# Performance work log

Hardware: AMD Instinct MI355X
Metric: run time of the kernel (lower is better)

The kernel has to match this reference:

```python
import jax, jax.numpy as jnp
import numpy as np

TOP_K = 8


def setup_inputs() -> dict:
    key = jax.random.key(0)
    k1, k2 = jax.random.split(key)
    N, D, E = 16384, 4096, 64
    x = jax.random.normal(k1, (N, D), dtype=jnp.float32)
    W = jax.random.normal(k2, (E, D), dtype=jnp.float32) * (1.0 / np.sqrt(D))
    b = jnp.zeros((E,), dtype=jnp.float32)
    return {"x": x, "W": W, "b": b}


def reference(x, W, b):
    # gate: [N, E]
    logits = jnp.einsum('nd,ed->ne', x, W) + b
    top_vals, top_idx = jax.lax.top_k(logits, TOP_K)  # [N, k]
    N = logits.shape[0]
    rows = jnp.arange(N)[:, None]  # [N, 1] broadcast against [N, k]
    neg_inf = jnp.full_like(logits, -jnp.inf)
    sparse = neg_inf.at[rows, top_idx].set(top_vals)
    sparse_logits = jax.nn.softmax(sparse, axis=-1)  # non-topk entries -> 0
    return (sparse_logits, top_idx)
```

## Files before the change

### kernel.cpp

```cpp
#include <hip/hip_runtime.h>
#include <cfloat>
#include <cmath>

#define M     16384
#define K     4096
#define E     64
#define TOPK  8
#define GAP_THRESH 1e-4f

#define SPLIT 4
#define KPS   (K / SPLIT)
#define NCH   (KPS / 32)
#define RCAP  2048
#define FKS   8

typedef __attribute__((ext_vector_type(8))) short bf16x8;
typedef __attribute__((ext_vector_type(4))) float f32x4;


__device__ __forceinline__ short f2bf(float f) {
    unsigned u = __builtin_bit_cast(unsigned, f);
    u += 0x7FFFu + ((u >> 16) & 1u);
    return (short)(u >> 16);
}
__device__ __forceinline__ float bf2f(short h) {
    unsigned u = ((unsigned)(unsigned short)h) << 16;
    return __builtin_bit_cast(float, u);
}

__global__ __launch_bounds__(256) void prep_kernel(const float* __restrict__ W,
                                                   short* __restrict__ Whf,
                                                   short* __restrict__ Wlf,
                                                   int* __restrict__ count) {
    int t = blockIdx.x * 256 + threadIdx.x;
    float w = W[t];
    short h = f2bf(w);
    short lo = f2bf(w - bf2f(h));
    int e = t >> 12, k = t & 4095;
    int gc = k >> 5, kk = k & 31;
    size_t fidx = (((size_t)gc * 4 + (e >> 4)) * 64 + (kk >> 3) * 16 + (e & 15)) * 8
                  + (kk & 7);
    Whf[fidx] = h;
    Wlf[fidx] = lo;
    if (t == 0) *count = 0;
}

struct XW {
    float4 xa, xb;
    bf16x8 h0, h1, h2, h3, l0, l1, l2, l3;
};

__device__ __forceinline__ void load_set(XW& s, const float* gx,
                                         const short* ph, const short* pl, int cc) {
    const int ko = cc * 32;
    s.xa = *reinterpret_cast<const float4*>(gx + ko);
    s.xb = *reinterpret_cast<const float4*>(gx + ko + 4);
    const short* bh = ph + (size_t)cc * 2048;
    const short* bl = pl + (size_t)cc * 2048;
    s.h0 = *reinterpret_cast<const bf16x8*>(bh);
    s.h1 = *reinterpret_cast<const bf16x8*>(bh + 512);
    s.h2 = *reinterpret_cast<const bf16x8*>(bh + 1024);
    s.h3 = *reinterpret_cast<const bf16x8*>(bh + 1536);
    s.l0 = *reinterpret_cast<const bf16x8*>(bl);
    s.l1 = *reinterpret_cast<const bf16x8*>(bl + 512);
    s.l2 = *reinterpret_cast<const bf16x8*>(bl + 1024);
    s.l3 = *reinterpret_cast<const bf16x8*>(bl + 1536);
}

__device__ __forceinline__ void compute_set(const XW& s, f32x4 acc[4]) {
    float vv[8] = {s.xa.x, s.xa.y, s.xa.z, s.xa.w, s.xb.x, s.xb.y, s.xb.z, s.xb.w};
    bf16x8 ah, al;
#pragma unroll
    for (int j = 0; j < 8; ++j) {
        short hh = f2bf(vv[j]);
        ah[j] = hh;
        al[j] = f2bf(vv[j] - bf2f(hh));
    }
    acc[0] = __builtin_amdgcn_mfma_f32_16x16x32_bf16(ah, s.h0, acc[0], 0, 0, 0);
    acc[0] = __builtin_amdgcn_mfma_f32_16x16x32_bf16(ah, s.l0, acc[0], 0, 0, 0);
    acc[0] = __builtin_amdgcn_mfma_f32_16x16x32_bf16(al, s.h0, acc[0], 0, 0, 0);
    acc[1] = __builtin_amdgcn_mfma_f32_16x16x32_bf16(ah, s.h1, acc[1], 0, 0, 0);
    acc[1] = __builtin_amdgcn_mfma_f32_16x16x32_bf16(ah, s.l1, acc[1], 0, 0, 0);
    acc[1] = __builtin_amdgcn_mfma_f32_16x16x32_bf16(al, s.h1, acc[1], 0, 0, 0);
    acc[2] = __builtin_amdgcn_mfma_f32_16x16x32_bf16(ah, s.h2, acc[2], 0, 0, 0);
    acc[2] = __builtin_amdgcn_mfma_f32_16x16x32_bf16(ah, s.l2, acc[2], 0, 0, 0);
    acc[2] = __builtin_amdgcn_mfma_f32_16x16x32_bf16(al, s.h2, acc[2], 0, 0, 0);
    acc[3] = __builtin_amdgcn_mfma_f32_16x16x32_bf16(ah, s.h3, acc[3], 0, 0, 0);
    acc[3] = __builtin_amdgcn_mfma_f32_16x16x32_bf16(ah, s.l3, acc[3], 0, 0, 0);
    acc[3] = __builtin_amdgcn_mfma_f32_16x16x32_bf16(al, s.h3, acc[3], 0, 0, 0);
}

__global__ __launch_bounds__(256) void gate_kernel(
    const float* __restrict__ x,
    const short* __restrict__ Whf,
    const short* __restrict__ Wlf,
    float* __restrict__ part)
{
    const int t  = threadIdx.x;
    const int l  = t & 63;
    const int wv = t >> 6;
    const int h    = blockIdx.x & (SPLIT - 1);
    const int row0 = (blockIdx.x >> 2) * 64 + wv * 16;
    const int k0   = h * KPS;

    const int kg   = l >> 4;
    const int xrow = row0 + (l & 15);

    const float* gx = x + (size_t)xrow * K + k0 + kg * 8;
    const short* ph = Whf + ((size_t)(k0 >> 5) * 4) * 512 + (size_t)l * 8;
    const short* pl = Wlf + ((size_t)(k0 >> 5) * 4) * 512 + (size_t)l * 8;

    f32x4 acc[4] = {{0,0,0,0},{0,0,0,0},{0,0,0,0},{0,0,0,0}};

    XW A, B;
    load_set(A, gx, ph, pl, 0);
    for (int c = 0; c < NCH; c += 2) {
        load_set(B, gx, ph, pl, c + 1);
        compute_set(A, acc);
        if (c + 2 < NCH) load_set(A, gx, ph, pl, c + 2);
        compute_set(B, acc);
    }

#pragma unroll
    for (int et = 0; et < 4; ++et)
#pragma unroll
        for (int r = 0; r < 4; ++r)
            part[((size_t)h * M + row0 + (l >> 4) * 4 + r) * E + et * 16 + (l & 15)]
                = acc[et][r];
}

__global__ __launch_bounds__(256) void reduce_kernel(
    const float* __restrict__ part,
    const float* __restrict__ b,
    float* __restrict__ outp,
    float* __restrict__ outi,
    int*   __restrict__ count,
    int*   __restrict__ list)
{
    const int lane = threadIdx.x & 63;
    const int w    = threadIdx.x >> 6;
    const int row  = blockIdx.x * 4 + w;

    float orig = b[lane];
#pragma unroll
    for (int hh = 0; hh < SPLIT; ++hh)
        orig += part[((size_t)hh * M + row) * E + lane];

    float cur = orig;
    float vals[9];
    float myidxf = 0.0f;
    bool  sel = false;

#pragma unroll
    for (int i = 0; i < 9; ++i) {
        float m = cur;
#pragma unroll
        for (int off = 32; off > 0; off >>= 1)
            m = fmaxf(m, __shfl_xor(m, off, 64));
        unsigned long long msk = __ballot(cur == m);
        int il = __ffsll((long long)msk) - 1;
        vals[i] = m;
        if (lane == il) { cur = -FLT_MAX; if (i < TOPK) sel = true; }
        if (i < TOPK && lane == i) myidxf = (float)il;
    }

    float ssum = 0.0f;
#pragma unroll
    for (int i = 0; i < TOPK; ++i) ssum += expf(vals[i] - vals[0]);
    float p = sel ? (expf(orig - vals[0]) / ssum) : 0.0f;

    outp[(size_t)row * E + lane] = p;
    if (lane < TOPK) outi[(size_t)row * TOPK + lane] = myidxf;

    float mingap = FLT_MAX;
#pragma unroll
    for (int i = 0; i < 8; ++i) mingap = fminf(mingap, vals[i] - vals[i + 1]);
    if (lane == 0 && mingap < GAP_THRESH) {
        int pos = atomicAdd(count, 1);
        if (pos < M) list[pos] = row;
    }
}

__global__ __launch_bounds__(256) void fix1_kernel(
    const float* __restrict__ x,
    const float* __restrict__ W,
    double* __restrict__ dsum,
    const int* __restrict__ count,
    const int* __restrict__ list)
{
    __shared__ float xsl[512];
    const int t   = threadIdx.x;
    const int l   = t & 63;
    const int wv  = t >> 6;
    const int tot = min(*count, RCAP) * FKS;

    for (int p = blockIdx.x; p < tot; p += gridDim.x) {
        const int i   = p >> 3;
        const int ks  = p & 7;
        const int row = list[i];
        const int k0  = ks << 9;

        if (t < 128)
            reinterpret_cast<float4*>(xsl)[t] =
                reinterpret_cast<const float4*>(x + (size_t)row * K + k0)[t];
        __syncthreads();

        const float4* xs4 = reinterpret_cast<const float4*>(xsl);

#pragma unroll
        for (int g = 0; g < 2; ++g) {
            const int e0 = wv * 16 + g * 8;
            float4 w0[8], w1[8];
#pragma unroll
            for (int e8 = 0; e8 < 8; ++e8) {
                const float4* wp = reinterpret_cast<const float4*>(
                    W + (size_t)(e0 + e8) * K + k0);
                w0[e8] = wp[l];
                w1[e8] = wp[l + 64];
            }
            float4 xv0 = xs4[l];
            float4 xv1 = xs4[l + 64];

            double s[8];
#pragma unroll
            for (int e8 = 0; e8 < 8; ++e8) {
                double a = 0.0;
                a = fma((double)xv0.x, (double)w0[e8].x, a);
                a = fma((double)xv0.y, (double)w0[e8].y, a);
                a = fma((double)xv0.z, (double)w0[e8].z, a);
                a = fma((double)xv0.w, (double)w0[e8].w, a);
                a = fma((double)xv1.x, (double)w1[e8].x, a);
                a = fma((double)xv1.y, (double)w1[e8].y, a);
                a = fma((double)xv1.z, (double)w1[e8].z, a);
                a = fma((double)xv1.w, (double)w1[e8].w, a);
                s[e8] = a;
            }

#pragma unroll
            for (int e8 = 0; e8 < 8; ++e8) {
                double v = s[e8];
#pragma unroll
                for (int off = 32; off > 0; off >>= 1)
                    v += __shfl_xor(v, off, 64);
                if (l == 0)
                    dsum[((size_t)i * FKS + ks) * E + e0 + e8] = v;
            }
        }
        __syncthreads();
    }
}

__global__ __launch_bounds__(64) void fix2_kernel(
    const double* __restrict__ dsum,
    const float*  __restrict__ b,
    float* __restrict__ outp,
    float* __restrict__ outi,
    const int* __restrict__ count,
    const int* __restrict__ list)
{
    const int l   = threadIdx.x;
    const int cnt = min(*count, RCAP);

    for (int i = blockIdx.x; i < cnt; i += gridDim.x) {
        const int row = list[i];

        double orig = (double)b[l];
#pragma unroll
        for (int ks = 0; ks < FKS; ++ks)
            orig += dsum[((size_t)i * FKS + ks) * E + l];

        double cur = orig;
        double vals[TOPK];
        float  myidxf = 0.0f;
        bool   sel = false;

#pragma unroll
        for (int tt = 0; tt < TOPK; ++tt) {
            double m = cur;
#pragma unroll
            for (int off = 32; off > 0; off >>= 1) {
                double o = __shfl_xor(m, off, 64);
                m = fmax(m, o);
            }
            unsigned long long msk = __ballot(cur == m);
            int il = __ffsll((long long)msk) - 1;
            vals[tt] = m;
            if (l == il) { cur = -DBL_MAX; sel = true; }
            if (l == tt)  myidxf = (float)il;
        }

        double ssum = 0.0;
#pragma unroll
        for (int tt = 0; tt < TOPK; ++tt) ssum += exp(vals[tt] - vals[0]);
        float p = sel ? (float)(exp(orig - vals[0]) / ssum) : 0.0f;

        outp[(size_t)row * E + l] = p;
        if (l < TOPK) outi[(size_t)row * TOPK + l] = myidxf;
    }
}

__global__ __launch_bounds__(64) void fallback_kernel(
    const float* __restrict__ x,
    const float* __restrict__ W,
    const float* __restrict__ b,
    float* __restrict__ outp,
    float* __restrict__ outi)
{
    const int row = blockIdx.x * 64 + threadIdx.x;
    double lg[64];
#pragma unroll
    for (int e = 0; e < 64; ++e) lg[e] = (double)b[e];
    const float* xr = x + (size_t)row * K;
    for (int k = 0; k < K; k += 4) {
        float4 xa = *reinterpret_cast<const float4*>(xr + k);
        double xd[4] = {(double)xa.x, (double)xa.y, (double)xa.z, (double)xa.w};
#pragma unroll
        for (int e = 0; e < 64; ++e) {
            const float* wp = W + (size_t)e * K + k;
            double a = lg[e];
#pragma unroll
            for (int j = 0; j < 4; ++j) a = fma(xd[j], (double)wp[j], a);
            lg[e] = a;
        }
    }
    unsigned long long selm = 0ull;
    double vals[TOPK]; int idx[TOPK];
#pragma unroll
    for (int i = 0; i < TOPK; ++i) {
        double m = -DBL_MAX; int mi = 0;
#pragma unroll
        for (int e = 0; e < 64; ++e) {
            bool gt = !((selm >> e) & 1ull) && (lg[e] > m);
            m = gt ? lg[e] : m; mi = gt ? e : mi;
        }
        vals[i] = m; idx[i] = mi; selm |= (1ull << mi);
    }
    double ssum = 0.0;
#pragma unroll
    for (int i = 0; i < TOPK; ++i) ssum += exp(vals[i] - vals[0]);
    double inv = 1.0 / ssum;
#pragma unroll
    for (int e = 0; e < 64; ++e)
        outp[(size_t)row * E + e] =
            ((selm >> e) & 1ull) ? (float)(exp(lg[e] - vals[0]) * inv) : 0.0f;
#pragma unroll
    for (int i = 0; i < TOPK; ++i)
        outi[(size_t)row * TOPK + i] = (float)idx[i];
}

extern "C" void kernel_launch(void* const* d_in, const int* in_sizes, int n_in,
                              void* d_out, int out_size, void* d_ws, size_t ws_size,
                              hipStream_t stream) {
    (void)in_sizes; (void)n_in; (void)out_size;
    const float* x = (const float*)d_in[0];
    const float* W = (const float*)d_in[1];
    const float* b = (const float*)d_in[2];

    float* outp = (float*)d_out;
    float* outi = outp + (size_t)M * E;

    const size_t wh_off   = 0;
    const size_t wl_off   = wh_off + sizeof(short) * (size_t)E * K;
    const size_t cnt_off  = wl_off + sizeof(short) * (size_t)E * K;
    const size_t list_off = cnt_off + 256;
    const size_t part_off = list_off + (size_t)M * sizeof(int);
    const size_t dsum_off = part_off + (size_t)SPLIT * M * E * sizeof(float);
    const size_t need     = dsum_off + (size_t)RCAP * FKS * E * sizeof(double);

    if (ws_size >= need) {
        short*  Whf  = (short*)((char*)d_ws + wh_off);
        short*  Wlf  = (short*)((char*)d_ws + wl_off);
        int*    cnt  = (int*)((char*)d_ws + cnt_off);
        int*    list = (int*)((char*)d_ws + list_off);
        float*  part = (float*)((char*)d_ws + part_off);
        double* dsum = (double*)((char*)d_ws + dsum_off);

        prep_kernel<<<(E * K) / 256, 256, 0, stream>>>(W, Whf, Wlf, cnt);
        gate_kernel<<<(M / 64) * SPLIT, 256, 0, stream>>>(x, Whf, Wlf, part);
        reduce_kernel<<<M / 4, 256, 0, stream>>>(part, b, outp, outi, cnt, list);
        fix1_kernel<<<4096, 256, 0, stream>>>(x, W, dsum, cnt, list);
        fix2_kernel<<<1024, 64, 0, stream>>>(dsum, b, outp, outi, cnt, list);
    } else {
        fallback_kernel<<<M / 64, 64, 0, stream>>>(x, W, b, outp, outi);
    }
}
```

Measured before the change: 127.3 us.

## Drop split-K and fuse top-k softmax reduction into gate kernel

The gate GEMM no longer splits K across four blocks; each block now accumulates the full K range for its 64 rows. The logits go to shared memory, and each wave runs the top-k, softmax and gap check on its own 16 rows inside the same kernel. This removes the partial-sum buffer round trip through global memory and one kernel launch. In exchange the grid shrinks from 1024 to 256 blocks, and each wave handles its 16 rows of top-k one after another, which lowers parallelism and latency hiding on the memory-bound read of x.

```diff
diff --git a/kernel.cpp b/kernel.cpp
--- a/kernel.cpp
+++ b/kernel.cpp
@@ -8,9 +8,7 @@
 #define TOPK  8
 #define GAP_THRESH 1e-4f
 
-#define SPLIT 4
-#define KPS   (K / SPLIT)
-#define NCH   (KPS / 32)
+#define NCH   (K / 32)
 #define RCAP  2048
 #define FKS   8
 
@@ -94,21 +92,25 @@
     const float* __restrict__ x,
     const short* __restrict__ Whf,
     const short* __restrict__ Wlf,
-    float* __restrict__ part)
+    const float* __restrict__ b,
+    float* __restrict__ outp,
+    float* __restrict__ outi,
+    int*   __restrict__ count,
+    int*   __restrict__ list)
 {
+    __shared__ float llog[64 * E];
+
     const int t  = threadIdx.x;
     const int l  = t & 63;
     const int wv = t >> 6;
-    const int h    = blockIdx.x & (SPLIT - 1);
-    const int row0 = (blockIdx.x >> 2) * 64 + wv * 16;
-    const int k0   = h * KPS;
+    const int row0 = blockIdx.x * 64 + wv * 16;
 
     const int kg   = l >> 4;
     const int xrow = row0 + (l & 15);
 
-    const float* gx = x + (size_t)xrow * K + k0 + kg * 8;
-    const short* ph = Whf + ((size_t)(k0 >> 5) * 4) * 512 + (size_t)l * 8;
-    const short* pl = Wlf + ((size_t)(k0 >> 5) * 4) * 512 + (size_t)l * 8;
+    const float* gx = x + (size_t)xrow * K + kg * 8;
+    const short* ph = Whf + (size_t)l * 8;
+    const short* pl = Wlf + (size_t)l * 8;
 
     f32x4 acc[4] = {{0,0,0,0},{0,0,0,0},{0,0,0,0},{0,0,0,0}};
 
@@ -125,59 +127,48 @@
     for (int et = 0; et < 4; ++et)
 #pragma unroll
         for (int r = 0; r < 4; ++r)
-            part[((size_t)h * M + row0 + (l >> 4) * 4 + r) * E + et * 16 + (l & 15)]
+            llog[((size_t)wv * 16 + (l >> 4) * 4 + r) * E + et * 16 + (l & 15)]
                 = acc[et][r];
-}
-
-__global__ __launch_bounds__(256) void reduce_kernel(
-    const float* __restrict__ part,
-    const float* __restrict__ b,
-    float* __restrict__ outp,
-    float* __restrict__ outi,
-    int*   __restrict__ count,
-    int*   __restrict__ list)
-{
-    const int lane = threadIdx.x & 63;
-    const int w    = threadIdx.x >> 6;
-    const int row  = blockIdx.x * 4 + w;
-
-    float orig = b[lane];
-#pragma unroll
-    for (int hh = 0; hh < SPLIT; ++hh)
-        orig += part[((size_t)hh * M + row) * E + lane];
-
-    float cur = orig;
-    float vals[9];
-    float myidxf = 0.0f;
-    bool  sel = false;
-
-#pragma unroll
-    for (int i = 0; i < 9; ++i) {
-        float m = cur;
-#pragma unroll
-        for (int off = 32; off > 0; off >>= 1)
-            m = fmaxf(m, __shfl_xor(m, off, 64));
-        unsigned long long msk = __ballot(cur == m);
-        int il = __ffsll((long long)msk) - 1;
-        vals[i] = m;
-        if (lane == il) { cur = -FLT_MAX; if (i < TOPK) sel = true; }
-        if (i < TOPK && lane == i) myidxf = (float)il;
-    }
-
-    float ssum = 0.0f;
-#pragma unroll
-    for (int i = 0; i < TOPK; ++i) ssum += expf(vals[i] - vals[0]);
-    float p = sel ? (expf(orig - vals[0]) / ssum) : 0.0f;
-
-    outp[(size_t)row * E + lane] = p;
-    if (lane < TOPK) outi[(size_t)row * TOPK + lane] = myidxf;
-
-    float mingap = FLT_MAX;
-#pragma unroll
-    for (int i = 0; i < 8; ++i) mingap = fminf(mingap, vals[i] - vals[i + 1]);
-    if (lane == 0 && mingap < GAP_THRESH) {
-        int pos = atomicAdd(count, 1);
-        if (pos < M) list[pos] = row;
+
+    const float bv = b[l];
+    for (int rr = 0; rr < 16; ++rr) {
+        const int rloc = wv * 16 + rr;
+        const int row  = blockIdx.x * 64 + rloc;
+        const float orig = llog[rloc * E + l] + bv;
+
+        float cur = orig;
+        float vals[9];
+        float myidxf = 0.0f;
+        bool  sel = false;
+
+#pragma unroll
+        for (int i = 0; i < 9; ++i) {
+            float m = cur;
+#pragma unroll
+            for (int off = 32; off > 0; off >>= 1)
+                m = fmaxf(m, __shfl_xor(m, off, 64));
+            unsigned long long msk = __ballot(cur == m);
+            int il = __ffsll((long long)msk) - 1;
+            vals[i] = m;
+            if (l == il) { cur = -FLT_MAX; if (i < TOPK) sel = true; }
+            if (i < TOPK && l == i) myidxf = (float)il;
+        }
+
+        float ssum = 0.0f;
+#pragma unroll
+        for (int i = 0; i < TOPK; ++i) ssum += expf(vals[i] - vals[0]);
+        float p = sel ? (expf(orig - vals[0]) / ssum) : 0.0f;
+
+        outp[(size_t)row * E + l] = p;
+        if (l < TOPK) outi[(size_t)row * TOPK + l] = myidxf;
+
+        float mingap = FLT_MAX;
+#pragma unroll
+        for (int i = 0; i < 8; ++i) mingap = fminf(mingap, vals[i] - vals[i + 1]);
+        if (l == 0 && mingap < GAP_THRESH) {
+            int pos = atomicAdd(count, 1);
+            if (pos < M) list[pos] = row;
+        }
     }
 }
 
@@ -363,8 +354,7 @@
     const size_t wl_off   = wh_off + sizeof(short) * (size_t)E * K;
     const size_t cnt_off  = wl_off + sizeof(short) * (size_t)E * K;
     const size_t list_off = cnt_off + 256;
-    const size_t part_off = list_off + (size_t)M * sizeof(int);
-    const size_t dsum_off = part_off + (size_t)SPLIT * M * E * sizeof(float);
+    const size_t dsum_off = list_off + (size_t)M * sizeof(int);
     const size_t need     = dsum_off + (size_t)RCAP * FKS * E * sizeof(double);
 
     if (ws_size >= need) {
@@ -372,12 +362,10 @@
         short*  Wlf  = (short*)((char*)d_ws + wl_off);
         int*    cnt  = (int*)((char*)d_ws + cnt_off);
         int*    list = (int*)((char*)d_ws + list_off);
-        float*  part = (float*)((char*)d_ws + part_off);
         double* dsum = (double*)((char*)d_ws + dsum_off);
 
         prep_kernel<<<(E * K) / 256, 256, 0, stream>>>(W, Whf, Wlf, cnt);
-        gate_kernel<<<(M / 64) * SPLIT, 256, 0, stream>>>(x, Whf, Wlf, part);
-        reduce_kernel<<<M / 4, 256, 0, stream>>>(part, b, outp, outi, cnt, list);
+        gate_kernel<<<M / 64, 256, 0, stream>>>(x, Whf, Wlf, b, outp, outi, cnt, list);
         fix1_kernel<<<4096, 256, 0, stream>>>(x, W, dsum, cnt, list);
         fix2_kernel<<<1024, 64, 0, stream>>>(dsum, b, outp, outi, cnt, list);
     } else {
```

After: 138.4 us. 8.7% more time.
